# Optimization experiments

Hardware: AMD Instinct MI355X
Metric: run time of the kernel (lower is better)

The kernel has to match this reference:

```python
import jax, jax.numpy as jnp
import numpy as np

B, S, F, H, E = 32, 2048, 16, 64, 256

def setup_inputs() -> dict:
    key = jax.random.key(0)
    ks = jax.random.split(key, 7)
    x = jax.random.normal(ks[0], (B, S, F), dtype=jnp.float32)
    masked_index = jax.random.randint(ks[1], (B, S, F), 0, 2) > 0
    W1 = jax.random.normal(ks[2], (F, H), dtype=jnp.float32) * 0.1
    b1 = jax.random.normal(ks[3], (F, H), dtype=jnp.float32) * 0.1
    W2 = jax.random.normal(ks[4], (F, E, H), dtype=jnp.float32) * 0.1
    b2 = jax.random.normal(ks[5], (F, E), dtype=jnp.float32) * 0.1
    masked_values = jax.random.normal(ks[6], (F, E), dtype=jnp.float32)
    return {"x": x, "masked_index": masked_index, "W1": W1, "b1": b1,
            "W2": W2, "b2": b2, "masked_values": masked_values}

def reference(x, masked_index, W1, b1, W2, b2, masked_values):
    # Per-feature 1->64 linear: x[...,None] * W1[f] + b1[f]  -> [B,S,F,H]
    h = jax.nn.gelu(x[..., None] * W1 + b1, approximate=False)
    # dropout is identity in eval mode
    # Per-feature 64->E linear (batched over F): [B,S,F,E]
    embeds = jnp.einsum('bsfh,feh->bsfe', h, W2) + b2
    # Replace masked positions with learned masked_values, then sum over features
    embeds = jnp.where(masked_index[..., None], masked_values, embeds)
    return jnp.sum(embeds, axis=-2)  # [B,S,E]
```

## Files before the change

kernel.cpp:

```cpp
#include <hip/hip_runtime.h>
#include <hip/hip_bf16.h>
#include <cstdint>
#include <math.h>


#define F_ 16
#define H_ 64
#define E_ 256
#define NT 256
#define BS_TOTAL 65536
#define XSCALE 6.0f
#define PI_F 3.14159265358979f

typedef __attribute__((ext_vector_type(8))) short s16x8;
typedef __attribute__((ext_vector_type(4))) float f32x4;

__device__ __forceinline__ unsigned short f2bf(float f){
  unsigned u = __builtin_bit_cast(unsigned, f);
  u += 0x7FFFu + ((u >> 16) & 1u);
  return (unsigned short)(u >> 16);
}
__device__ __forceinline__ unsigned cvtpk(float a, float b){
  unsigned r; asm("v_cvt_pk_bf16_f32 %0, %1, %2" : "=v"(r) : "v"(a), "v"(b)); return r;
}

__global__ __launch_bounds__(256)
void prep_cmat(const float* __restrict__ W1, const float* __restrict__ b1,
               const float* __restrict__ W2, const float* __restrict__ b2,
               const float* __restrict__ mv, unsigned short* __restrict__ Cmat){
  const int f = blockIdx.x >> 3, eg = blockIdx.x & 7;
  const int t = threadIdx.x;
  __shared__ float hs[16][H_];
  __shared__ float ct[14][16];
  __shared__ float ph_s[32][17];

  #pragma unroll
  for (int s = 0; s < 4; ++s){
    int idx = t + s * 256;
    int j = idx >> 6, h = idx & 63;
    float xj = XSCALE * cosf(PI_F * (j + 0.5f) / 16.0f);
    float z = fmaf(xj, W1[f * H_ + h], b1[f * H_ + h]);
    hs[j][h] = 0.5f * z * (1.0f + erff(z * 0.7071067811865475f));
  }
  if (t < 224){
    int d = t >> 4, j = t & 15;
    ct[d][j] = cosf(PI_F * (d + 1) * (j + 0.5f) / 16.0f) * 0.125f;
  }
  __syncthreads();

  {
    const int e_l = t & 31, jp = t >> 5;
    const int e = eg * 32 + e_l;
    const int j0 = jp * 2, j1 = j0 + 1;
    const float4* w2p = (const float4*)(W2 + ((long)f * E_ + e) * H_);
    float b2v = b2[f * E_ + e];
    float p0 = b2v, p1 = b2v;
    #pragma unroll
    for (int hq = 0; hq < 16; ++hq){
      float4 w  = w2p[hq];
      float4 h0 = *(const float4*)&hs[j0][hq * 4];
      float4 h1 = *(const float4*)&hs[j1][hq * 4];
      p0 += w.x * h0.x + w.y * h0.y + w.z * h0.z + w.w * h0.w;
      p1 += w.x * h1.x + w.y * h1.y + w.z * h1.z + w.w * h1.w;
    }
    ph_s[e_l][j0] = p0; ph_s[e_l][j1] = p1;
  }
  __syncthreads();

  if (t < 64){
    const int el = t & 31, g = t >> 5;
    const int ee = eg * 32 + el;
    float ph[16]; float s0 = 0.f;
    #pragma unroll
    for (int j = 0; j < 16; ++j){ ph[j] = ph_s[el][j]; s0 += ph[j]; }
    float c0 = s0 * 0.0625f;
    float vals[8];
    #pragma unroll
    for (int dq = 0; dq < 8; ++dq){
      int dm = g * 8 + dq;
      float v;
      if (dm < 14){
        v = 0.f;
        #pragma unroll
        for (int j = 0; j < 16; ++j) v += ph[j] * ct[dm][j];
      } else if (dm == 14) v = mv[f * E_ + ee] - c0;
      else                 v = c0;
      vals[dq] = v;
    }
    unsigned w[4];
    w[0] = (unsigned)f2bf(vals[0]) | ((unsigned)f2bf(vals[1]) << 16);
    w[1] = (unsigned)f2bf(vals[2]) | ((unsigned)f2bf(vals[3]) << 16);
    w[2] = (unsigned)f2bf(vals[4]) | ((unsigned)f2bf(vals[5]) << 16);
    w[3] = (unsigned)f2bf(vals[6]) | ((unsigned)f2bf(vals[7]) << 16);
    const int kk = g * 4 + (f & 3);
    const int lane = (f >> 2) * 16 + (ee & 15);
    const int eb = ee >> 4;
    long byte = ((long)(kk * 16 + eb) * 64 + lane) * 16;
    *(uint4*)((char*)Cmat + byte) = *(uint4*)w;
  }
}

__global__ __launch_bounds__(NT, 3)
void ts_main(const float* __restrict__ x, const int* __restrict__ mask,
             const unsigned short* __restrict__ Cmat, float* __restrict__ out){
  const int tid = threadIdx.x, lane = tid & 63, wn = tid >> 6;
  const int rr = lane & 15;
  const int q  = lane >> 4;
  const int rowBase = blockIdx.x * 64;

  float4 x4[4]; unsigned mbits = 0;
  #pragma unroll
  for (int m = 0; m < 4; ++m){
    int r = rowBase + m * 16 + rr;
    x4[m] = *(const float4*)&x[r * F_ + q * 4];
    int4 mk = *(const int4*)&mask[r * F_ + q * 4];
    mbits |= (mk.x != 0 ? 1u : 0u) << (m * 4 + 0);
    mbits |= (mk.y != 0 ? 1u : 0u) << (m * 4 + 1);
    mbits |= (mk.z != 0 ? 1u : 0u) << (m * 4 + 2);
    mbits |= (mk.w != 0 ? 1u : 0u) << (m * 4 + 3);
  }

  const s16x8* C8 = (const s16x8*)Cmat;
  f32x4 acc[4][4] = {};

  #pragma unroll
  for (int c = 0; c < 4; ++c){
    float t2s[4], T7s[4], T8s[4];

    {
      s16x8 bfr[4];
      #pragma unroll
      for (int n = 0; n < 4; ++n)
        bfr[n] = C8[(c * 16 + wn * 4 + n) * 64 + lane];
      s16x8 afr[4];
      #pragma unroll
      for (int m = 0; m < 4; ++m){
        float xv = ((const float*)&x4[m])[c];
        unsigned masked = (mbits >> (m * 4 + c)) & 1u;
        float uu = xv * (1.0f / XSCALE);
        uu = fminf(1.0f, fmaxf(-1.0f, uu));
        float t2 = uu + uu;
        float T1 = uu;
        float T2 = fmaf(t2, T1, -1.0f);
        float T3 = fmaf(t2, T2, -T1);
        float T4 = fmaf(t2, T3, -T2);
        float T5 = fmaf(t2, T4, -T3);
        float T6 = fmaf(t2, T5, -T4);
        float T7 = fmaf(t2, T6, -T5);
        float T8 = fmaf(t2, T7, -T6);
        t2s[m] = t2; T7s[m] = T7; T8s[m] = T8;
        unsigned z = masked ? 0u : 0xFFFFFFFFu;
        union { unsigned w[4]; s16x8 v; } pk;
        pk.w[0] = cvtpk(T1, T2) & z;  pk.w[1] = cvtpk(T3, T4) & z;
        pk.w[2] = cvtpk(T5, T6) & z;  pk.w[3] = cvtpk(T7, T8) & z;
        afr[m] = pk.v;
      }
      #pragma unroll
      for (int m = 0; m < 4; ++m)
        #pragma unroll
        for (int n = 0; n < 4; ++n)
          acc[m][n] = __builtin_amdgcn_mfma_f32_16x16x32_bf16(bfr[n], afr[m], acc[m][n], 0, 0, 0);
    }

    {
      s16x8 bfr[4];
      #pragma unroll
      for (int n = 0; n < 4; ++n)
        bfr[n] = C8[((c + 4) * 16 + wn * 4 + n) * 64 + lane];
      s16x8 afr[4];
      #pragma unroll
      for (int m = 0; m < 4; ++m){
        unsigned masked = (mbits >> (m * 4 + c)) & 1u;
        float t2 = t2s[m], T7 = T7s[m], T8 = T8s[m];
        float T9  = fmaf(t2, T8,  -T7);
        float T10 = fmaf(t2, T9,  -T8);
        float T11 = fmaf(t2, T10, -T9);
        float T12 = fmaf(t2, T11, -T10);
        float T13 = fmaf(t2, T12, -T11);
        float T14 = fmaf(t2, T13, -T12);
        unsigned z = masked ? 0u : 0xFFFFFFFFu;
        float mf = masked ? 1.0f : 0.0f;
        union { unsigned w[4]; s16x8 v; } pk;
        pk.w[0] = cvtpk(T9, T10) & z;  pk.w[1] = cvtpk(T11, T12) & z;
        pk.w[2] = cvtpk(T13, T14) & z; pk.w[3] = cvtpk(mf, 1.0f);
        afr[m] = pk.v;
      }
      #pragma unroll
      for (int m = 0; m < 4; ++m)
        #pragma unroll
        for (int n = 0; n < 4; ++n)
          acc[m][n] = __builtin_amdgcn_mfma_f32_16x16x32_bf16(bfr[n], afr[m], acc[m][n], 0, 0, 0);
    }
  }

  #pragma unroll
  for (int m = 0; m < 4; ++m){
    int r = rowBase + m * 16 + (lane & 15);
    #pragma unroll
    for (int n = 0; n < 4; ++n){
      int e = wn * 64 + n * 16 + (lane >> 4) * 4;
      __builtin_nontemporal_store(acc[m][n], (f32x4*)&out[(long)r * E_ + e]);
    }
  }
}

extern "C" void kernel_launch(void* const* d_in, const int* in_sizes, int n_in,
                              void* d_out, int out_size, void* d_ws, size_t ws_size,
                              hipStream_t stream) {
  const float* x    = (const float*)d_in[0];
  const int*   mask = (const int*)d_in[1];
  const float* W1   = (const float*)d_in[2];
  const float* b1   = (const float*)d_in[3];
  const float* W2   = (const float*)d_in[4];
  const float* b2   = (const float*)d_in[5];
  const float* mv   = (const float*)d_in[6];
  float* out = (float*)d_out;

  unsigned short* Cmat = (unsigned short*)d_ws;

  prep_cmat<<<dim3(128), dim3(256), 0, stream>>>(W1, b1, W2, b2, mv, Cmat);
  ts_main<<<dim3(BS_TOTAL / 64), dim3(NT), 0, stream>>>(x, mask, Cmat, out);
}
```

Baseline: 31.84 us.

## Stage output tile through swizzled LDS for row-contiguous coalesced stores

Accumulator fragments are written to a 16x256 shared-memory tile with an XOR swizzle, then read back so each wave writes full contiguous 1KB output rows with nontemporal stores, in place of scattered 16-byte stores. MFMA issue is interleaved with A-fragment generation per m, removing the afr array, and launch bounds are raised to 4 waves per SIMD. This targets write coalescing on the output, which at 64MB dominates traffic. It adds 16KB of LDS per block and two barriers per m-step, and the tighter register budget may cause spills.

```diff
diff --git a/kernel.cpp b/kernel.cpp
--- a/kernel.cpp
+++ b/kernel.cpp
@@ -9,6 +9,7 @@
 #define E_ 256
 #define NT 256
 #define BS_TOTAL 65536
+#define BM 64
 #define XSCALE 6.0f
 #define PI_F 3.14159265358979f
 
@@ -100,13 +101,16 @@
   }
 }
 
-__global__ __launch_bounds__(NT, 3)
+__global__ __launch_bounds__(NT, 4)
 void ts_main(const float* __restrict__ x, const int* __restrict__ mask,
              const unsigned short* __restrict__ Cmat, float* __restrict__ out){
+  __shared__ __align__(16) float osm[16 * E_];
+
   const int tid = threadIdx.x, lane = tid & 63, wn = tid >> 6;
   const int rr = lane & 15;
   const int q  = lane >> 4;
-  const int rowBase = blockIdx.x * 64;
+  const int rowBase = blockIdx.x * BM;
+  const s16x8* C8 = (const s16x8*)Cmat;
 
   float4 x4[4]; unsigned mbits = 0;
   #pragma unroll
@@ -120,7 +124,6 @@
     mbits |= (mk.w != 0 ? 1u : 0u) << (m * 4 + 3);
   }
 
-  const s16x8* C8 = (const s16x8*)Cmat;
   f32x4 acc[4][4] = {};
 
   #pragma unroll
@@ -132,7 +135,6 @@
       #pragma unroll
       for (int n = 0; n < 4; ++n)
         bfr[n] = C8[(c * 16 + wn * 4 + n) * 64 + lane];
-      s16x8 afr[4];
       #pragma unroll
       for (int m = 0; m < 4; ++m){
         float xv = ((const float*)&x4[m])[c];
@@ -153,13 +155,10 @@
         union { unsigned w[4]; s16x8 v; } pk;
         pk.w[0] = cvtpk(T1, T2) & z;  pk.w[1] = cvtpk(T3, T4) & z;
         pk.w[2] = cvtpk(T5, T6) & z;  pk.w[3] = cvtpk(T7, T8) & z;
-        afr[m] = pk.v;
-      }
-      #pragma unroll
-      for (int m = 0; m < 4; ++m)
         #pragma unroll
         for (int n = 0; n < 4; ++n)
-          acc[m][n] = __builtin_amdgcn_mfma_f32_16x16x32_bf16(bfr[n], afr[m], acc[m][n], 0, 0, 0);
+          acc[m][n] = __builtin_amdgcn_mfma_f32_16x16x32_bf16(bfr[n], pk.v, acc[m][n], 0, 0, 0);
+      }
     }
 
     {
@@ -167,7 +166,6 @@
       #pragma unroll
       for (int n = 0; n < 4; ++n)
         bfr[n] = C8[((c + 4) * 16 + wn * 4 + n) * 64 + lane];
-      s16x8 afr[4];
       #pragma unroll
       for (int m = 0; m < 4; ++m){
         unsigned masked = (mbits >> (m * 4 + c)) & 1u;
@@ -183,24 +181,31 @@
         union { unsigned w[4]; s16x8 v; } pk;
         pk.w[0] = cvtpk(T9, T10) & z;  pk.w[1] = cvtpk(T11, T12) & z;
         pk.w[2] = cvtpk(T13, T14) & z; pk.w[3] = cvtpk(mf, 1.0f);
-        afr[m] = pk.v;
-      }
-      #pragma unroll
-      for (int m = 0; m < 4; ++m)
         #pragma unroll
         for (int n = 0; n < 4; ++n)
-          acc[m][n] = __builtin_amdgcn_mfma_f32_16x16x32_bf16(bfr[n], afr[m], acc[m][n], 0, 0, 0);
+          acc[m][n] = __builtin_amdgcn_mfma_f32_16x16x32_bf16(bfr[n], pk.v, acc[m][n], 0, 0, 0);
+      }
     }
   }
 
   #pragma unroll
   for (int m = 0; m < 4; ++m){
-    int r = rowBase + m * 16 + (lane & 15);
     #pragma unroll
     for (int n = 0; n < 4; ++n){
-      int e = wn * 64 + n * 16 + (lane >> 4) * 4;
-      __builtin_nontemporal_store(acc[m][n], (f32x4*)&out[(long)r * E_ + e]);
-    }
+      int byte = (rr * E_ + wn * 64 + n * 16 + q * 4) * 4;
+      byte ^= (rr & 7) << 4;
+      *(f32x4*)((char*)osm + byte) = acc[m][n];
+    }
+    __syncthreads();
+    #pragma unroll
+    for (int i = 0; i < 4; ++i){
+      int row = wn * 4 + i;
+      int byte = (row * E_ + lane * 4) * 4;
+      byte ^= (row & 7) << 4;
+      f32x4 v = *(const f32x4*)((const char*)osm + byte);
+      __builtin_nontemporal_store(v, (f32x4*)&out[(long)(rowBase + m * 16 + row) * E_ + lane * 4]);
+    }
+    __syncthreads();
   }
 }
 
@@ -219,5 +224,5 @@
   unsigned short* Cmat = (unsigned short*)d_ws;
 
   prep_cmat<<<dim3(128), dim3(256), 0, stream>>>(W1, b1, W2, b2, mv, Cmat);
-  ts_main<<<dim3(BS_TOTAL / 64), dim3(NT), 0, stream>>>(x, mask, Cmat, out);
-}
+  ts_main<<<dim3(BS_TOTAL / BM), dim3(NT), 0, stream>>>(x, mask, Cmat, out);
+}
```

Result: faster. 30.05 us (-5.6%).
